# Kernel tuning notes

Hardware: AMD Instinct MI355X
Metric: run time of the kernel (lower is better)

The kernel has to match this reference:

```python
import jax, jax.numpy as jnp
import numpy as np

NUM_HEADS = 12
HEAD_DIM = 64
EPS = 1e-6


def rms_norm(x, w):
    # normalize over last dim (head_dim)
    norm = jax.lax.rsqrt(jnp.mean(x * x, axis=-1, keepdims=True) + EPS)
    return x * norm * w


def apply_rotary_emb(x, cos, sin):
    x1, x2 = jnp.split(x, 2, axis=-1)
    return jnp.concatenate([x1 * cos - x2 * sin, x2 * cos + x1 * sin], axis=-1)


def setup_inputs() -> dict:
    key = jax.random.key(0)
    ks = jax.random.split(key, 6)
    B, N, C = 4, 2048, 768
    return {
        "x": jax.random.normal(ks[0], (B, N, C), dtype=jnp.float32),
        "cos": jax.random.uniform(ks[1], (1, 1, N, HEAD_DIM // 2), dtype=jnp.float32),
        "sin": jax.random.uniform(ks[2], (1, 1, N, HEAD_DIM // 2), dtype=jnp.float32),
        "qkv_w": jax.random.normal(ks[3], (3 * C, C), dtype=jnp.float32) * (C ** -0.5),
        "q_norm_w": jnp.ones((HEAD_DIM,), dtype=jnp.float32),
        "k_norm_w": jnp.ones((HEAD_DIM,), dtype=jnp.float32),
        "proj_w": jax.random.normal(ks[4], (C, C), dtype=jnp.float32) * (C ** -0.5),
        "proj_b": jnp.zeros((C,), dtype=jnp.float32),
    }


def reference(x, cos, sin, qkv_w, q_norm_w, k_norm_w, proj_w, proj_b):
    B, N, C = x.shape
    H, D = NUM_HEADS, HEAD_DIM
    scale = D ** -0.5
    # qkv projection: [B,N,3C] -> [3,B,H,N,D]
    qkv = jnp.einsum('bnc,oc->bno', x, qkv_w)
    qkv = qkv.reshape(B, N, 3, H, D).transpose(2, 0, 3, 1, 4)
    q, k, v = qkv[0], qkv[1], qkv[2]
    q = rms_norm(q, q_norm_w)
    k = rms_norm(k, k_norm_w)
    q = apply_rotary_emb(q, cos, sin)
    k = apply_rotary_emb(k, cos, sin)
    attn = jnp.einsum('bhqd,bhkd->bhqk', q, k) * scale
    attn = jax.nn.softmax(attn, axis=-1)
    out = jnp.einsum('bhqk,bhkd->bhqd', attn, v)
    out = out.transpose(0, 2, 1, 3).reshape(B, N, C)
    out = jnp.einsum('bnc,oc->bno', out, proj_w) + proj_b
    return out
```

## Files before the change

### kernel.cpp

```cpp
#include <hip/hip_runtime.h>
#include <hip/hip_bf16.h>

#define BB 4
#define NN 2048
#define CC 768
#define HH 12
#define DD 64

typedef __bf16 bf16;
typedef __attribute__((ext_vector_type(8))) __bf16 bf16x8;
typedef __attribute__((ext_vector_type(4))) __bf16 bf16x4;
typedef __attribute__((ext_vector_type(4))) float f32x4;

#define SZ_X    (BB * NN * CC)
#define SZ_QKVW (3 * CC * CC)
#define SZ_PW   (CC * CC)
#define SZ_QKV  ((size_t)BB * NN * 3 * CC)

#define OFF_X    0
#define OFF_QW   (OFF_X + SZ_X)
#define OFF_PW   (OFF_QW + SZ_QKVW)
#define OFF_QKV  (OFF_PW + SZ_PW)

__device__ __forceinline__ void async16(const bf16* g, bf16* l) {
    __builtin_amdgcn_global_load_lds(
        (const __attribute__((address_space(1))) unsigned int*)g,
        (__attribute__((address_space(3))) unsigned int*)l, 16, 0, 0);
}

__device__ __forceinline__ void cast8(const float* __restrict__ src,
                                      bf16* __restrict__ dst, int i) {
    f32x4 a = ((const f32x4*)src)[2 * i];
    f32x4 b = ((const f32x4*)src)[2 * i + 1];
    bf16x8 o;
#pragma unroll
    for (int j = 0; j < 4; ++j) { o[j] = (bf16)a[j]; o[j + 4] = (bf16)b[j]; }
    ((bf16x8*)dst)[i] = o;
}

__global__ __launch_bounds__(256) void convert3(
    const float* __restrict__ x, const float* __restrict__ qkvw,
    const float* __restrict__ pw, bf16* __restrict__ ws) {
    const int t = blockIdx.x * 256 + threadIdx.x;
    const int S = gridDim.x * 256;
    for (int i = t; i < SZ_X / 8;    i += S) cast8(x,    ws + OFF_X,  i);
    for (int i = t; i < SZ_QKVW / 8; i += S) cast8(qkvw, ws + OFF_QW, i);
    for (int i = t; i < SZ_PW / 8;   i += S) cast8(pw,   ws + OFF_PW, i);
}

__global__ __launch_bounds__(256) void gemm_qkv(
    const bf16* __restrict__ A, const bf16* __restrict__ W,
    bf16* __restrict__ C, bf16* __restrict__ Vt,
    const float* __restrict__ cosb, const float* __restrict__ sinb,
    const float* __restrict__ qw, const float* __restrict__ kw) {
    __shared__ __align__(16) bf16 As[128 * 64];
    __shared__ __align__(16) bf16 Bs[128 * 64];
    const int tid  = threadIdx.x;
    const int wave = tid >> 6;
    const int lane = tid & 63;
    const int quad = lane >> 4;
    const int l16  = lane & 15;
    const int m0 = blockIdx.y * 128;
    const int n0 = blockIdx.x * 128;
    const int wm = (wave >> 1) * 64;
    const int wn = (wave & 1) * 64;
    const int srow = lane >> 3;
    const int swz  = (lane & 7) ^ srow;
    const int K = CC;
    const int Nn = 3 * CC;

    f32x4 acc[4][4];
#pragma unroll
    for (int i = 0; i < 4; ++i)
#pragma unroll
        for (int j = 0; j < 4; ++j) acc[i][j] = (f32x4){0.f, 0.f, 0.f, 0.f};

    for (int k0 = 0; k0 < K; k0 += 64) {
#pragma unroll
        for (int i = 0; i < 4; ++i) {
            int row = i * 32 + wave * 8 + srow;
            async16(A + (size_t)(m0 + row) * CC + k0 + swz * 8,
                    &As[(i * 32 + wave * 8) * 64]);
            async16(W + (size_t)(n0 + row) * K + k0 + swz * 8,
                    &Bs[(i * 32 + wave * 8) * 64]);
        }
        __syncthreads();
#pragma unroll
        for (int kk = 0; kk < 2; ++kk) {
            const int slot = ((kk * 4 + quad) ^ (l16 & 7)) * 8;
            bf16x8 af[4], bf[4];
#pragma unroll
            for (int mt = 0; mt < 4; ++mt)
                af[mt] = *(const bf16x8*)(&As[(wm + mt * 16 + l16) * 64 + slot]);
#pragma unroll
            for (int nt = 0; nt < 4; ++nt)
                bf[nt] = *(const bf16x8*)(&Bs[(wn + nt * 16 + l16) * 64 + slot]);
#pragma unroll
            for (int mt = 0; mt < 4; ++mt)
#pragma unroll
                for (int nt = 0; nt < 4; ++nt)
                    acc[mt][nt] = __builtin_amdgcn_mfma_f32_16x16x32_bf16(
                        af[mt], bf[nt], acc[mt][nt], 0, 0, 0);
        }
        __syncthreads();
    }

    const int colblk = n0 + wn;
    const int sector = colblk / CC;
    if (sector == 2) {
        const int head = (colblk >> 6) - 24;
        const int btok = m0 + wm;
        const int bh   = (btok >> 11) * HH + head;
        const int nloc = btok & (NN - 1);
#pragma unroll
        for (int nt = 0; nt < 4; ++nt) {
            const int d = nt * 16 + l16;
            bf16* dst = Vt + ((size_t)bh * DD + d) * NN + nloc + quad * 4;
#pragma unroll
            for (int mt = 0; mt < 4; ++mt) {
                bf16x4 pk;
#pragma unroll
                for (int r = 0; r < 4; ++r) pk[r] = (bf16)acc[mt][nt][r];
                *(bf16x4*)(dst + mt * 16) = pk;
            }
        }
    } else {
        const float* wp = (sector == 0) ? qw : kw;
        const float qs = (sector == 0) ? 0.18033688f : 1.0f;
        float wv[4];
#pragma unroll
        for (int nt = 0; nt < 4; ++nt) wv[nt] = wp[nt * 16 + l16];
#pragma unroll
        for (int mt = 0; mt < 4; ++mt)
#pragma unroll
            for (int r = 0; r < 4; ++r) {
                const int row = m0 + wm + mt * 16 + quad * 4 + r;
                const int n   = row & (NN - 1);
                float v[4];
#pragma unroll
                for (int nt = 0; nt < 4; ++nt) v[nt] = acc[mt][nt][r];
                float ss = v[0] * v[0] + v[1] * v[1] + v[2] * v[2] + v[3] * v[3];
                ss += __shfl_xor(ss, 1, 64);
                ss += __shfl_xor(ss, 2, 64);
                ss += __shfl_xor(ss, 4, 64);
                ss += __shfl_xor(ss, 8, 64);
                const float rn = rsqrtf(ss * (1.0f / 64.0f) + 1e-6f);
#pragma unroll
                for (int nt = 0; nt < 4; ++nt) v[nt] *= rn * wv[nt];
                const float c0 = cosb[n * 32 + l16];
                const float c1 = cosb[n * 32 + 16 + l16];
                const float s0 = sinb[n * 32 + l16];
                const float s1 = sinb[n * 32 + 16 + l16];
                float y[4];
                y[0] = v[0] * c0 - v[2] * s0;
                y[1] = v[1] * c1 - v[3] * s1;
                y[2] = v[2] * c0 + v[0] * s0;
                y[3] = v[3] * c1 + v[1] * s1;
#pragma unroll
                for (int nt = 0; nt < 4; ++nt) {
                    int col = colblk + nt * 16 + l16;
                    C[(size_t)row * Nn + col] = (bf16)(y[nt] * qs);
                }
            }
    }
}

__global__ __launch_bounds__(256) void gemm_proj(
    const bf16* __restrict__ A, const bf16* __restrict__ W,
    const float* __restrict__ bias, float* __restrict__ C) {
    __shared__ __align__(16) bf16 As[128 * 64];
    __shared__ __align__(16) bf16 Bs[64 * 64];
    const int tid  = threadIdx.x;
    const int wave = tid >> 6;
    const int lane = tid & 63;
    const int quad = lane >> 4;
    const int l16  = lane & 15;
    const int m0 = blockIdx.y * 128;
    const int n0 = blockIdx.x * 64;
    const int wm = (wave >> 1) * 64;
    const int wn = (wave & 1) * 32;
    const int srow = lane >> 3;
    const int swz  = (lane & 7) ^ srow;
    const int lda = 3 * CC;
    const int K = CC;

    f32x4 acc[4][2];
#pragma unroll
    for (int i = 0; i < 4; ++i)
#pragma unroll
        for (int j = 0; j < 2; ++j) acc[i][j] = (f32x4){0.f, 0.f, 0.f, 0.f};

    for (int k0 = 0; k0 < K; k0 += 64) {
#pragma unroll
        for (int i = 0; i < 4; ++i) {
            int row = i * 32 + wave * 8 + srow;
            async16(A + (size_t)(m0 + row) * lda + k0 + swz * 8,
                    &As[(i * 32 + wave * 8) * 64]);
        }
#pragma unroll
        for (int i = 0; i < 2; ++i) {
            int row = i * 32 + wave * 8 + srow;
            async16(W + (size_t)(n0 + row) * K + k0 + swz * 8,
                    &Bs[(i * 32 + wave * 8) * 64]);
        }
        __syncthreads();
#pragma unroll
        for (int kk = 0; kk < 2; ++kk) {
            const int slot = ((kk * 4 + quad) ^ (l16 & 7)) * 8;
            bf16x8 af[4], bf[2];
#pragma unroll
            for (int mt = 0; mt < 4; ++mt)
                af[mt] = *(const bf16x8*)(&As[(wm + mt * 16 + l16) * 64 + slot]);
#pragma unroll
            for (int nt = 0; nt < 2; ++nt)
                bf[nt] = *(const bf16x8*)(&Bs[(wn + nt * 16 + l16) * 64 + slot]);
#pragma unroll
            for (int mt = 0; mt < 4; ++mt)
#pragma unroll
                for (int nt = 0; nt < 2; ++nt)
                    acc[mt][nt] = __builtin_amdgcn_mfma_f32_16x16x32_bf16(
                        af[mt], bf[nt], acc[mt][nt], 0, 0, 0);
        }
        __syncthreads();
    }
#pragma unroll
    for (int mt = 0; mt < 4; ++mt)
#pragma unroll
        for (int nt = 0; nt < 2; ++nt)
#pragma unroll
            for (int r = 0; r < 4; ++r) {
                int row = m0 + wm + mt * 16 + quad * 4 + r;
                int col = n0 + wn + nt * 16 + l16;
                C[(size_t)row * CC + col] = acc[mt][nt][r] + bias[col];
            }
}

__global__ __launch_bounds__(512) void flash_attn(
    const bf16* __restrict__ qkv, const bf16* __restrict__ Vt,
    bf16* __restrict__ Oqkv) {
    __shared__ __align__(16) bf16 Ks[2][64 * 64];
    __shared__ __align__(16) bf16 Vs[2][64 * 64];
    __shared__ __align__(16) bf16 Ps[8][32 * 72];
    const int tid  = threadIdx.x;
    const int wave = tid >> 6;
    const int w4   = wave & 3;
    const int half = wave >> 2;
    const int lane = tid & 63;
    const int quad = lane >> 4;
    const int l16  = lane & 15;
    const int r7   = l16 & 7;
    const int bh = blockIdx.x;
    const int qt = blockIdx.y;
    const int b = bh / HH, h = bh % HH;
    const size_t rs = 3 * CC;
    const bf16* Qb  = qkv + (size_t)b * NN * rs + h * DD;
    const bf16* Kb  = Qb + CC;
    const bf16* Vtb = Vt + (size_t)bh * DD * NN;

    bf16x8 qf[2][2];
#pragma unroll
    for (int f = 0; f < 2; ++f) {
        const int qrow = qt * 128 + w4 * 32 + f * 16 + l16;
#pragma unroll
        for (int hf = 0; hf < 2; ++hf)
            qf[f][hf] = *(const bf16x8*)(Qb + (size_t)qrow * rs + hf * 32 + quad * 8);
    }

    f32x4 accO[2][4];
#pragma unroll
    for (int f = 0; f < 2; ++f)
#pragma unroll
        for (int i = 0; i < 4; ++i) accO[f][i] = (f32x4){0.f, 0.f, 0.f, 0.f};
    float lsum[2] = {0.f, 0.f};

    const int srow  = lane >> 3;
    const int swz   = (lane & 7) ^ srow;
    const int strow = wave * 8 + srow;

    for (int step = 0; step < NN / 128; ++step) {
        const int t0 = step * 2;
        async16(Kb + (size_t)(t0 * 64 + strow) * rs + swz * 8,
                &Ks[0][(wave * 8) * 64]);
        async16(Kb + (size_t)((t0 + 1) * 64 + strow) * rs + swz * 8,
                &Ks[1][(wave * 8) * 64]);
        async16(Vtb + (size_t)strow * NN + t0 * 64 + swz * 8,
                &Vs[0][(wave * 8) * 64]);
        async16(Vtb + (size_t)strow * NN + (t0 + 1) * 64 + swz * 8,
                &Vs[1][(wave * 8) * 64]);
        __syncthreads();

        const bf16* Kc = Ks[half];
        const bf16* Vc = Vs[half];

        f32x4 s[2][4];
#pragma unroll
        for (int nt = 0; nt < 4; ++nt) {
            const int row = nt * 16 + l16;
            bf16x8 kf0 = *(const bf16x8*)(&Kc[row * 64 + (quad ^ r7) * 8]);
            bf16x8 kf1 = *(const bf16x8*)(&Kc[row * 64 + ((quad + 4) ^ r7) * 8]);
#pragma unroll
            for (int f = 0; f < 2; ++f) {
                f32x4 z = (f32x4){0.f, 0.f, 0.f, 0.f};
                z = __builtin_amdgcn_mfma_f32_16x16x32_bf16(kf0, qf[f][0], z, 0, 0, 0);
                s[f][nt] = __builtin_amdgcn_mfma_f32_16x16x32_bf16(kf1, qf[f][1], z, 0, 0, 0);
            }
        }

#pragma unroll
        for (int f = 0; f < 2; ++f)
#pragma unroll
            for (int nt = 0; nt < 4; ++nt) {
                bf16x4 pk;
#pragma unroll
                for (int r = 0; r < 4; ++r) {
                    float pv = __builtin_amdgcn_exp2f(s[f][nt][r]);
                    lsum[f] += pv;
                    pk[r] = (bf16)pv;
                }
                *(bf16x4*)(&Ps[wave][(f * 16 + l16) * 72 + nt * 16 + quad * 4]) = pk;
            }
        __asm__ volatile("s_waitcnt lgkmcnt(0)" ::: "memory");

        bf16x8 pf0[2], pf1[2];
#pragma unroll
        for (int f = 0; f < 2; ++f) {
            pf0[f] = *(const bf16x8*)(&Ps[wave][(f * 16 + l16) * 72 + quad * 8]);
            pf1[f] = *(const bf16x8*)(&Ps[wave][(f * 16 + l16) * 72 + 32 + quad * 8]);
        }
#pragma unroll
        for (int nt = 0; nt < 4; ++nt) {
            const int rowd = nt * 16 + l16;
            bf16x8 vf0 = *(const bf16x8*)(&Vc[rowd * 64 + (quad ^ r7) * 8]);
            bf16x8 vf1 = *(const bf16x8*)(&Vc[rowd * 64 + ((quad + 4) ^ r7) * 8]);
#pragma unroll
            for (int f = 0; f < 2; ++f) {
                accO[f][nt] = __builtin_amdgcn_mfma_f32_16x16x32_bf16(pf0[f], vf0, accO[f][nt], 0, 0, 0);
                accO[f][nt] = __builtin_amdgcn_mfma_f32_16x16x32_bf16(pf1[f], vf1, accO[f][nt], 0, 0, 0);
            }
        }
        __syncthreads();
    }

#pragma unroll
    for (int f = 0; f < 2; ++f) {
        lsum[f] += __shfl_xor(lsum[f], 16, 64);
        lsum[f] += __shfl_xor(lsum[f], 32, 64);
    }

    float* Osc = (float*)&Ps[0][0];
    float* Ls  = Osc + 4 * 32 * 65;
    if (wave >= 4) {
#pragma unroll
        for (int f = 0; f < 2; ++f) {
            if (quad == 0) Ls[w4 * 32 + f * 16 + l16] = lsum[f];
#pragma unroll
            for (int nt = 0; nt < 4; ++nt)
#pragma unroll
                for (int r = 0; r < 4; ++r)
                    Osc[(w4 * 32 + f * 16 + quad * 4 + r) * 65 + nt * 16 + l16] =
                        accO[f][nt][r];
        }
    }
    __syncthreads();
    if (wave < 4) {
#pragma unroll
        for (int f = 0; f < 2; ++f) {
            lsum[f] += Ls[w4 * 32 + f * 16 + l16];
#pragma unroll
            for (int nt = 0; nt < 4; ++nt)
#pragma unroll
                for (int r = 0; r < 4; ++r)
                    accO[f][nt][r] +=
                        Osc[(w4 * 32 + f * 16 + quad * 4 + r) * 65 + nt * 16 + l16];
        }
#pragma unroll
        for (int f = 0; f < 2; ++f)
#pragma unroll
            for (int r = 0; r < 4; ++r) {
                float inv = 1.0f / __shfl(lsum[f], quad * 4 + r, 64);
                int n = qt * 128 + w4 * 32 + f * 16 + quad * 4 + r;
#pragma unroll
                for (int nt = 0; nt < 4; ++nt) {
                    int col = h * DD + nt * 16 + l16;
                    Oqkv[(size_t)(b * NN + n) * rs + 2 * CC + col] =
                        (bf16)(accO[f][nt][r] * inv);
                }
            }
    }
}

extern "C" void kernel_launch(void* const* d_in, const int* in_sizes, int n_in,
                              void* d_out, int out_size, void* d_ws, size_t ws_size,
                              hipStream_t stream) {
    const float* x     = (const float*)d_in[0];
    const float* cosb  = (const float*)d_in[1];
    const float* sinb  = (const float*)d_in[2];
    const float* qkv_w = (const float*)d_in[3];
    const float* qnw   = (const float*)d_in[4];
    const float* knw   = (const float*)d_in[5];
    const float* pw    = (const float*)d_in[6];
    const float* pb    = (const float*)d_in[7];
    float* out = (float*)d_out;

    bf16* ws  = (bf16*)d_ws;
    bf16* xb  = ws + OFF_X;
    bf16* qwb = ws + OFF_QW;
    bf16* pwb = ws + OFF_PW;
    bf16* qkv = ws + OFF_QKV;
    bf16* vt  = (bf16*)d_out;

    const int M = BB * NN;

    convert3<<<1024, 256, 0, stream>>>(x, qkv_w, pw, ws);

    dim3 g1(3 * CC / 128, M / 128);
    gemm_qkv<<<g1, 256, 0, stream>>>(xb, qwb, qkv, vt, cosb, sinb, qnw, knw);

    dim3 g4(BB * HH, NN / 128);
    flash_attn<<<g4, 512, 0, stream>>>(qkv, vt, qkv);

    dim3 g5(CC / 64, M / 128);
    gemm_proj<<<g5, 256, 0, stream>>>(qkv + 2 * CC, pwb, pb, out);
}
```

Baseline: 231.1 us.

## Keep attention probabilities in registers by permuting V transpose layout

The V-transpose store in the QKV epilogue now uses a permuted key order, so the MFMA output layout of the exp'd scores matches the A-operand layout needed for the P·V MFMA. This removes the per-wave LDS staging buffer for P, along with its write, wait and reload in every key tile. The end-of-kernel cross-half reduction reuses the K/V shared buffers in two passes, which shrinks LDS use and may raise occupancy but adds extra barriers. Correctness depends on the Q·K score order matching the permuted V order, since sums over keys are order-invariant.

```diff
diff --git a/kernel.cpp b/kernel.cpp
--- a/kernel.cpp
+++ b/kernel.cpp
@@ -115,13 +115,13 @@
 #pragma unroll
         for (int nt = 0; nt < 4; ++nt) {
             const int d = nt * 16 + l16;
-            bf16* dst = Vt + ((size_t)bh * DD + d) * NN + nloc + quad * 4;
+            bf16* dst = Vt + ((size_t)bh * DD + d) * NN + nloc + quad * 8;
 #pragma unroll
             for (int mt = 0; mt < 4; ++mt) {
                 bf16x4 pk;
 #pragma unroll
                 for (int r = 0; r < 4; ++r) pk[r] = (bf16)acc[mt][nt][r];
-                *(bf16x4*)(dst + mt * 16) = pk;
+                *(bf16x4*)(dst + (mt >> 1) * 32 + (mt & 1) * 4) = pk;
             }
         }
     } else {
@@ -240,7 +240,6 @@
     bf16* __restrict__ Oqkv) {
     __shared__ __align__(16) bf16 Ks[2][64 * 64];
     __shared__ __align__(16) bf16 Vs[2][64 * 64];
-    __shared__ __align__(16) bf16 Ps[8][32 * 72];
     const int tid  = threadIdx.x;
     const int wave = tid >> 6;
     const int w4   = wave & 3;
@@ -306,27 +305,19 @@
             }
         }
 
+        bf16x8 pfa[2], pfb[2];
 #pragma unroll
         for (int f = 0; f < 2; ++f)
 #pragma unroll
-            for (int nt = 0; nt < 4; ++nt) {
-                bf16x4 pk;
+            for (int nt = 0; nt < 4; ++nt)
 #pragma unroll
                 for (int r = 0; r < 4; ++r) {
                     float pv = __builtin_amdgcn_exp2f(s[f][nt][r]);
                     lsum[f] += pv;
-                    pk[r] = (bf16)pv;
+                    if (nt < 2) pfa[f][nt * 4 + r] = (bf16)pv;
+                    else        pfb[f][(nt - 2) * 4 + r] = (bf16)pv;
                 }
-                *(bf16x4*)(&Ps[wave][(f * 16 + l16) * 72 + nt * 16 + quad * 4]) = pk;
-            }
-        __asm__ volatile("s_waitcnt lgkmcnt(0)" ::: "memory");
-
-        bf16x8 pf0[2], pf1[2];
-#pragma unroll
-        for (int f = 0; f < 2; ++f) {
-            pf0[f] = *(const bf16x8*)(&Ps[wave][(f * 16 + l16) * 72 + quad * 8]);
-            pf1[f] = *(const bf16x8*)(&Ps[wave][(f * 16 + l16) * 72 + 32 + quad * 8]);
-        }
+
 #pragma unroll
         for (int nt = 0; nt < 4; ++nt) {
             const int rowd = nt * 16 + l16;
@@ -334,8 +325,8 @@
             bf16x8 vf1 = *(const bf16x8*)(&Vc[rowd * 64 + ((quad + 4) ^ r7) * 8]);
 #pragma unroll
             for (int f = 0; f < 2; ++f) {
-                accO[f][nt] = __builtin_amdgcn_mfma_f32_16x16x32_bf16(pf0[f], vf0, accO[f][nt], 0, 0, 0);
-                accO[f][nt] = __builtin_amdgcn_mfma_f32_16x16x32_bf16(pf1[f], vf1, accO[f][nt], 0, 0, 0);
+                accO[f][nt] = __builtin_amdgcn_mfma_f32_16x16x32_bf16(pfa[f], vf0, accO[f][nt], 0, 0, 0);
+                accO[f][nt] = __builtin_amdgcn_mfma_f32_16x16x32_bf16(pfb[f], vf1, accO[f][nt], 0, 0, 0);
             }
         }
         __syncthreads();
@@ -347,37 +338,31 @@
         lsum[f] += __shfl_xor(lsum[f], 32, 64);
     }
 
-    float* Osc = (float*)&Ps[0][0];
-    float* Ls  = Osc + 4 * 32 * 65;
-    if (wave >= 4) {
-#pragma unroll
-        for (int f = 0; f < 2; ++f) {
+    float* Osc = (float*)&Ks[0][0];
+    float* Ls  = Osc + 64 * 68;
+#pragma unroll
+    for (int f = 0; f < 2; ++f) {
+        if (wave >= 4) {
             if (quad == 0) Ls[w4 * 32 + f * 16 + l16] = lsum[f];
 #pragma unroll
             for (int nt = 0; nt < 4; ++nt)
 #pragma unroll
                 for (int r = 0; r < 4; ++r)
-                    Osc[(w4 * 32 + f * 16 + quad * 4 + r) * 65 + nt * 16 + l16] =
+                    Osc[(w4 * 16 + quad * 4 + r) * 68 + nt * 16 + l16] =
                         accO[f][nt][r];
         }
-    }
-    __syncthreads();
-    if (wave < 4) {
-#pragma unroll
-        for (int f = 0; f < 2; ++f) {
-            lsum[f] += Ls[w4 * 32 + f * 16 + l16];
+        __syncthreads();
+        if (wave < 4) {
+            float lt = lsum[f] + Ls[w4 * 32 + f * 16 + l16];
 #pragma unroll
             for (int nt = 0; nt < 4; ++nt)
 #pragma unroll
                 for (int r = 0; r < 4; ++r)
                     accO[f][nt][r] +=
-                        Osc[(w4 * 32 + f * 16 + quad * 4 + r) * 65 + nt * 16 + l16];
-        }
-#pragma unroll
-        for (int f = 0; f < 2; ++f)
+                        Osc[(w4 * 16 + quad * 4 + r) * 68 + nt * 16 + l16];
 #pragma unroll
             for (int r = 0; r < 4; ++r) {
-                float inv = 1.0f / __shfl(lsum[f], quad * 4 + r, 64);
+                float inv = 1.0f / __shfl(lt, quad * 4 + r, 64);
                 int n = qt * 128 + w4 * 32 + f * 16 + quad * 4 + r;
 #pragma unroll
                 for (int nt = 0; nt < 4; ++nt) {
@@ -386,6 +371,8 @@
                         (bf16)(accO[f][nt][r] * inv);
                 }
             }
+        }
+        __syncthreads();
     }
 }
 
```

Result: faster. 224.3 us (-2.9%).
